# Kernel optimization log

Hardware: AMD Instinct MI355X
Metric: run time of the kernel (lower is better)

## Reference

```python
import jax, jax.numpy as jnp
import numpy as np

T, N, C, D, K = 512, 256, 128, 128, 128

def setup_inputs() -> dict:
    key = jax.random.key(0)
    ks = jax.random.split(key, 6)
    s = 1.0 / np.sqrt(D)
    return {
        "x":   jax.random.normal(ks[0], (T, N, C), dtype=jnp.float32),
        "W_x": jax.random.normal(ks[1], (D, C), dtype=jnp.float32) * s,  # torch Linear: (out,in)
        "b_x": jax.random.normal(ks[2], (D,), dtype=jnp.float32) * s,
        "W_h": jax.random.normal(ks[3], (D, D), dtype=jnp.float32) * s,
        "W_y": jax.random.normal(ks[4], (K, D), dtype=jnp.float32) * s,
        "b_y": jax.random.normal(ks[5], (K,), dtype=jnp.float32) * s,
    }

def reference(x, W_x, b_x, W_h, W_y, b_y):
    # Elman RNN: h_t = relu(x_t @ W_x^T + b_x + h_{t-1} @ W_h^T)
    # Precompute the input projection for all timesteps in one big GEMM,
    # then scan only the true recurrent dependency.
    xproj = jnp.einsum('tnc,dc->tnd', x, W_x) + b_x  # (T, N, D)

    def step(h, xp_t):
        h_new = jax.nn.relu(xp_t + h @ W_h.T)  # (N, D)
        return h_new, h_new

    h0 = jnp.zeros((x.shape[1], W_h.shape[0]), dtype=x.dtype)
    _, all_h = jax.lax.scan(step, h0, xproj)          # (T, N, D)
    all_y = jnp.einsum('tnd,kd->tnk', all_h, W_y) + b_y  # (T, N, K)
    return all_y, all_h
```

## Files before the change

kernel.cpp:

```cpp
#include <hip/hip_runtime.h>

static constexpr int T_STEPS = 512;
static constexpr int NBATCH  = 256;
static constexpr int DD      = 128;
static constexpr long TND    = (long)T_STEPS * NBATCH * DD;

typedef short bf16x8 __attribute__((ext_vector_type(8)));
typedef float f32x4  __attribute__((ext_vector_type(4)));
typedef unsigned u32x4 __attribute__((ext_vector_type(4)));

__device__ inline unsigned short f2bf(float f) {
  unsigned u = __builtin_bit_cast(unsigned, f);
  unsigned r = u + 0x7FFFu + ((u >> 16) & 1u);
  return (unsigned short)(r >> 16);
}

__device__ inline bf16x8 pack8(const float* s) {
  bf16x8 v;
#pragma unroll
  for (int i = 0; i < 8; ++i) v[i] = (short)f2bf(s[i]);
  return v;
}

__device__ __forceinline__ unsigned cvtpk_bf16(float lo, float hi) {
  unsigned r;
  asm("v_cvt_pk_bf16_f32 %0, %1, %2" : "=v"(r) : "v"(lo), "v"(hi));
  return r;
}

__global__ __launch_bounds__(256) void gemm128_mfma(
    const float* __restrict__ A, const float* __restrict__ W,
    const float* __restrict__ bias, float* __restrict__ O, int ntiles) {
  const int lane = threadIdx.x & 63;
  const int wib  = threadIdx.x >> 6;
  const int m    = lane & 15;
  const int q    = lane >> 4;

  bf16x8 Wf[8][4];
#pragma unroll
  for (int j = 0; j < 8; ++j)
#pragma unroll
    for (int kq = 0; kq < 4; ++kq) {
      const float* p = W + (j * 16 + m) * DD + kq * 32 + q * 8;
      float t[8];
      *(float4*)&t[0] = *(const float4*)p;
      *(float4*)&t[4] = *(const float4*)(p + 4);
      Wf[j][kq] = pack8(t);
    }
  float bv[8];
#pragma unroll
  for (int j = 0; j < 8; ++j) bv[j] = bias[j * 16 + m];

  const int wglobal = blockIdx.x * 4 + wib;
  const int nwaves  = gridDim.x * 4;
  for (int tile = wglobal; tile < ntiles; tile += nwaves) {
    const long r0 = (long)tile * 16;
    f32x4 acc[8];
#pragma unroll
    for (int j = 0; j < 8; ++j) acc[j] = (f32x4){0.f, 0.f, 0.f, 0.f};

#pragma unroll
    for (int kq = 0; kq < 4; ++kq) {
      const float* p = A + (r0 + m) * DD + kq * 32 + q * 8;
      float t[8];
      *(float4*)&t[0] = *(const float4*)p;
      *(float4*)&t[4] = *(const float4*)(p + 4);
      bf16x8 af = pack8(t);
#pragma unroll
      for (int j = 0; j < 8; ++j)
        acc[j] = __builtin_amdgcn_mfma_f32_16x16x32_bf16(af, Wf[j][kq], acc[j], 0, 0, 0);
    }
#pragma unroll
    for (int j = 0; j < 8; ++j)
#pragma unroll
      for (int r = 0; r < 4; ++r)
        O[(r0 + q * 4 + r) * DD + j * 16 + m] = acc[j][r] + bv[j];
  }
}

__global__ __launch_bounds__(64, 1) void rnn_scan_mfma(
    const float* __restrict__ Wh, float* __restrict__ H ) {
  const int lane = threadIdx.x & 63;
  const int m = lane & 15;
  const int q = lane >> 4;

  bf16x8 Whf[8][4];
#pragma unroll
  for (int j = 0; j < 8; ++j)
#pragma unroll
    for (int kq = 0; kq < 4; ++kq) {
      const float* p = Wh + (j * 16 + m) * DD + kq * 32 + 4 * q;
      float t[8];
      *(float4*)&t[0] = *(const float4*)p;
      *(float4*)&t[4] = *(const float4*)(p + 16);
      Whf[j][kq] = pack8(t);
    }

  const long stepN = (long)NBATCH * DD;
  float* base = H + (long)(blockIdx.x * 16 + m) * DD + 4 * q;

  unsigned w[8][2];
#pragma unroll
  for (int j = 0; j < 8; ++j) { w[j][0] = 0u; w[j][1] = 0u; }

  auto pref = [&](f32x4 (&xp)[8], int t) {
    const float* pp = base + (long)t * stepN;
#pragma unroll
    for (int j = 0; j < 8; ++j) xp[j] = *(const f32x4*)(pp + j * 16);
  };

  auto step = [&](const f32x4 (&xp)[8], int t) {
    f32x4 acc[8];
#pragma unroll
    for (int j = 0; j < 8; ++j) acc[j] = xp[j];
#pragma unroll
    for (int kq = 0; kq < 4; ++kq) {
      u32x4 bw;
      bw[0] = w[2 * kq][0];     bw[1] = w[2 * kq][1];
      bw[2] = w[2 * kq + 1][0]; bw[3] = w[2 * kq + 1][1];
      bf16x8 bf = __builtin_bit_cast(bf16x8, bw);
#pragma unroll
      for (int j = 0; j < 8; ++j)
        acc[j] = __builtin_amdgcn_mfma_f32_16x16x32_bf16(Whf[j][kq], bf, acc[j], 0, 0, 0);
    }
    float* hp = base + (long)t * stepN;
#pragma unroll
    for (int j = 0; j < 8; ++j) {
      f32x4 hv;
#pragma unroll
      for (int r = 0; r < 4; ++r) hv[r] = fmaxf(acc[j][r], 0.f);
      w[j][0] = cvtpk_bf16(hv[0], hv[1]);
      w[j][1] = cvtpk_bf16(hv[2], hv[3]);
      *(f32x4*)(hp + j * 16) = hv;
    }
  };

  f32x4 xA[8], xB[8], xC[8], xD[8];
  pref(xA, 0); pref(xB, 1); pref(xC, 2); pref(xD, 3);

#pragma unroll 1
  for (int t = 0; t < T_STEPS; t += 4) {
    step(xA, t);     pref(xA, t + 4 < T_STEPS ? t + 4 : T_STEPS - 1);
    step(xB, t + 1); pref(xB, t + 5 < T_STEPS ? t + 5 : T_STEPS - 1);
    step(xC, t + 2); pref(xC, t + 6 < T_STEPS ? t + 6 : T_STEPS - 1);
    step(xD, t + 3); pref(xD, t + 7 < T_STEPS ? t + 7 : T_STEPS - 1);
  }
}

extern "C" void kernel_launch(void* const* d_in, const int* in_sizes, int n_in,
                              void* d_out, int out_size, void* d_ws, size_t ws_size,
                              hipStream_t stream) {
  const float* x  = (const float*)d_in[0];
  const float* Wx = (const float*)d_in[1];
  const float* bx = (const float*)d_in[2];
  const float* Wh = (const float*)d_in[3];
  const float* Wy = (const float*)d_in[4];
  const float* by = (const float*)d_in[5];

  float* Y = (float*)d_out;
  float* H = (float*)d_out + TND;

  const int ntiles = T_STEPS * NBATCH / 16;

  gemm128_mfma<<<512, 256, 0, stream>>>(x, Wx, bx, H, ntiles);
  rnn_scan_mfma<<<NBATCH / 16, 64, 0, stream>>>(Wh, H);
  gemm128_mfma<<<512, 256, 0, stream>>>(H, Wy, by, Y, ntiles);
}
```

Baseline: 542.4 us.

## Fuse input projection GEMM into the recurrent scan kernel

```diff
diff --git a/kernel.cpp b/kernel.cpp
--- a/kernel.cpp
+++ b/kernel.cpp
@@ -78,12 +78,26 @@
   }
 }
 
-__global__ __launch_bounds__(64, 1) void rnn_scan_mfma(
-    const float* __restrict__ Wh, float* __restrict__ H ) {
+__global__ __launch_bounds__(64, 1) void rnn_scan_fused(
+    const float* __restrict__ x,  const float* __restrict__ Wx,
+    const float* __restrict__ bx, const float* __restrict__ Wh,
+    float* __restrict__ H ) {
   const int lane = threadIdx.x & 63;
   const int m = lane & 15;
   const int q = lane >> 4;
 
+  bf16x8 Wxf[8][4];
+#pragma unroll
+  for (int j = 0; j < 8; ++j)
+#pragma unroll
+    for (int kq = 0; kq < 4; ++kq) {
+      const float* p = Wx + (j * 16 + m) * DD + kq * 32 + q * 8;
+      float t[8];
+      *(float4*)&t[0] = *(const float4*)p;
+      *(float4*)&t[4] = *(const float4*)(p + 4);
+      Wxf[j][kq] = pack8(t);
+    }
+
   bf16x8 Whf[8][4];
 #pragma unroll
   for (int j = 0; j < 8; ++j)
@@ -96,23 +110,47 @@
       Whf[j][kq] = pack8(t);
     }
 
+  f32x4 bxv[8];
+#pragma unroll
+  for (int j = 0; j < 8; ++j) bxv[j] = *(const f32x4*)(bx + j * 16 + 4 * q);
+
   const long stepN = (long)NBATCH * DD;
-  float* base = H + (long)(blockIdx.x * 16 + m) * DD + 4 * q;
+  const float* xb = x + (long)(blockIdx.x * 16 + m) * DD + 8 * q;
+  float*       hb = H + (long)(blockIdx.x * 16 + m) * DD + 4 * q;
 
   unsigned w[8][2];
 #pragma unroll
   for (int j = 0; j < 8; ++j) { w[j][0] = 0u; w[j][1] = 0u; }
 
-  auto pref = [&](f32x4 (&xp)[8], int t) {
-    const float* pp = base + (long)t * stepN;
-#pragma unroll
-    for (int j = 0; j < 8; ++j) xp[j] = *(const f32x4*)(pp + j * 16);
+  auto pref = [&](f32x4 (&r)[8], int t) {
+    const float* p = xb + (long)t * stepN;
+#pragma unroll
+    for (int kq = 0; kq < 4; ++kq) {
+      r[2 * kq]     = *(const f32x4*)(p + kq * 32);
+      r[2 * kq + 1] = *(const f32x4*)(p + kq * 32 + 4);
+    }
   };
 
-  auto step = [&](const f32x4 (&xp)[8], int t) {
+  auto step = [&](const f32x4 (&r)[8], int t) {
+    bf16x8 xf[4];
+#pragma unroll
+    for (int kq = 0; kq < 4; ++kq) {
+      u32x4 u;
+      u[0] = cvtpk_bf16(r[2 * kq][0],     r[2 * kq][1]);
+      u[1] = cvtpk_bf16(r[2 * kq][2],     r[2 * kq][3]);
+      u[2] = cvtpk_bf16(r[2 * kq + 1][0], r[2 * kq + 1][1]);
+      u[3] = cvtpk_bf16(r[2 * kq + 1][2], r[2 * kq + 1][3]);
+      xf[kq] = __builtin_bit_cast(bf16x8, u);
+    }
     f32x4 acc[8];
 #pragma unroll
-    for (int j = 0; j < 8; ++j) acc[j] = xp[j];
+    for (int j = 0; j < 8; ++j)
+      acc[j] = __builtin_amdgcn_mfma_f32_16x16x32_bf16(Wxf[j][0], xf[0], bxv[j], 0, 0, 0);
+#pragma unroll
+    for (int kq = 1; kq < 4; ++kq)
+#pragma unroll
+      for (int j = 0; j < 8; ++j)
+        acc[j] = __builtin_amdgcn_mfma_f32_16x16x32_bf16(Wxf[j][kq], xf[kq], acc[j], 0, 0, 0);
 #pragma unroll
     for (int kq = 0; kq < 4; ++kq) {
       u32x4 bw;
@@ -123,12 +161,12 @@
       for (int j = 0; j < 8; ++j)
         acc[j] = __builtin_amdgcn_mfma_f32_16x16x32_bf16(Whf[j][kq], bf, acc[j], 0, 0, 0);
     }
-    float* hp = base + (long)t * stepN;
+    float* hp = hb + (long)t * stepN;
 #pragma unroll
     for (int j = 0; j < 8; ++j) {
       f32x4 hv;
 #pragma unroll
-      for (int r = 0; r < 4; ++r) hv[r] = fmaxf(acc[j][r], 0.f);
+      for (int rr = 0; rr < 4; ++rr) hv[rr] = fmaxf(acc[j][rr], 0.f);
       w[j][0] = cvtpk_bf16(hv[0], hv[1]);
       w[j][1] = cvtpk_bf16(hv[2], hv[3]);
       *(f32x4*)(hp + j * 16) = hv;
@@ -162,7 +200,6 @@
 
   const int ntiles = T_STEPS * NBATCH / 16;
 
-  gemm128_mfma<<<512, 256, 0, stream>>>(x, Wx, bx, H, ntiles);
-  rnn_scan_mfma<<<NBATCH / 16, 64, 0, stream>>>(Wh, H);
+  rnn_scan_fused<<<NBATCH / 16, 64, 0, stream>>>(x, Wx, bx, Wh, H);
   gemm128_mfma<<<512, 256, 0, stream>>>(H, Wy, by, Y, ntiles);
 }
```

Measured after the change: 639.0 us. 17.8% more time.
